# Kernel tuning notes

Measured on AMD Instinct MI355X. Metric: run time of the kernel, lower is better.

Reference implementation:

```python
import jax, jax.numpy as jnp
import numpy as np

IN_F = 4096
OUT_F = 8192
BLOCK = 16   # block_dim
KEEP = 8     # keep_k low-frequency modes kept per block
NLEV = 256   # n_levels


def dct_inv_basis(keep_k, n):
    # Orthonormal DCT-II synthesis basis, rows = kept frequencies k, cols = time index t.
    k = jnp.arange(keep_k, dtype=jnp.float32)[:, None]
    t = jnp.arange(n, dtype=jnp.float32)[None, :]
    B = jnp.cos(jnp.pi * (t + 0.5) * k / n) * jnp.sqrt(2.0 / n)
    scale = jnp.where(jnp.arange(keep_k) == 0, 1.0 / jnp.sqrt(2.0), 1.0)
    return B * scale[:, None]  # [keep_k, block_dim]


def setup_inputs() -> dict:
    key = jax.random.key(0)
    k1, k2, k3, k4, k5 = jax.random.split(key, 5)
    n_blocks = OUT_F * IN_F // BLOCK  # 2097152
    x = jax.random.normal(k1, (32, 8, IN_F), jnp.float32)
    idx = jax.random.randint(k2, (n_blocks, KEEP), 0, NLEV, jnp.int32)
    c_min = jax.random.normal(k3, (KEEP,), jnp.float32)
    c_range = jax.random.uniform(k4, (KEEP,), jnp.float32) + 0.1
    bias = jax.random.normal(k5, (OUT_F,), jnp.float32)
    return {"x": x, "idx": idx, "c_min": c_min, "c_range": c_range, "bias": bias}


def reference(x, idx, c_min, c_range, bias):
    # Affine dequant of kept frequency codes: [n_blocks, keep_k]
    coeffs = idx.astype(jnp.float32) / (NLEV - 1) * c_range + c_min
    # Inverse DCT per block (high-frequency modes are implicitly zero)
    B = dct_inv_basis(KEEP, BLOCK)              # [keep_k, block_dim]
    W = (coeffs @ B).reshape(OUT_F, IN_F)       # dense dequantized weight
    return x @ W.T + bias
```

## Files before the change

kernel.cpp:

```cpp
#include <hip/hip_runtime.h>


typedef __attribute__((ext_vector_type(8))) short bf16x8;
typedef __attribute__((ext_vector_type(4))) float f32x4;

#define K_TOT   2048
#define N_TOT   8192
#define NT      32
#define NCHUNK  8
#define SPC     8
#define LDS_CH  16384

__device__ __forceinline__ unsigned short f2bf_rn(float f) {
    unsigned u = __float_as_uint(f);
    u += 0x7FFFu + ((u >> 16) & 1u);
    return (unsigned short)(u >> 16);
}
__device__ __forceinline__ unsigned pack2(int a, int b) {
    unsigned ua = __float_as_uint((float)a);
    unsigned ub = __float_as_uint((float)b);
    return __builtin_amdgcn_perm(ub, ua, 0x07060302u);
}

__device__ __forceinline__ void lds_barrier() {
    asm volatile("" ::: "memory");
    __builtin_amdgcn_s_waitcnt(0xC07F);
    __builtin_amdgcn_s_barrier();
    asm volatile("" ::: "memory");
}

__global__ __launch_bounds__(256) void prep_kernel(
    const float* __restrict__ x, const float* __restrict__ c_min,
    const float* __restrict__ c_range, unsigned short* __restrict__ Y2f,
    float* __restrict__ corr)
{
    __shared__ float Bk[8][16];
    __shared__ float scmin[8];
    __shared__ float ss[8];
    __shared__ float red[4];
    const int tid = threadIdx.x;
    const int m = blockIdx.x;
    if (tid < 128) {
        int k = tid >> 4, t = tid & 15;
        float v = cosf(3.14159265358979f * (t + 0.5f) * (float)k / 16.0f)
                  * 0.353553390593274f;
        if (k == 0) v *= 0.707106781186548f;
        Bk[k][t] = v;
    }
    if (tid < 8) {
        scmin[tid] = c_min[tid];
        ss[tid] = c_range[tid] * (1.0f / 255.0f);
    }
    __syncthreads();

    const float* xp = x + (long)m * 4096 + tid * 16;
    float xs[16];
#pragma unroll
    for (int q = 0; q < 4; ++q) {
        float4 v = *(const float4*)(xp + q * 4);
        xs[q * 4 + 0] = v.x; xs[q * 4 + 1] = v.y;
        xs[q * 4 + 2] = v.z; xs[q * 4 + 3] = v.w;
    }
    float partial = 0.0f;
    unsigned short yo[8];
#pragma unroll
    for (int k = 0; k < 8; ++k) {
        float y = 0.0f;
#pragma unroll
        for (int t = 0; t < 16; ++t) y += xs[t] * Bk[k][t];
        partial += y * scmin[k];
        yo[k] = f2bf_rn(y * ss[k]);
    }
    uint4 pk;
    pk.x = (unsigned)yo[0] | ((unsigned)yo[1] << 16);
    pk.y = (unsigned)yo[2] | ((unsigned)yo[3] << 16);
    pk.z = (unsigned)yo[4] | ((unsigned)yo[5] << 16);
    pk.w = (unsigned)yo[6] | ((unsigned)yo[7] << 16);
    {
        const int mg = m >> 4, fr = m & 15, kc = tid >> 2, fq = tid & 3;
        unsigned short* dst = Y2f + ((long)((mg * 64 + kc) * 64) + fq * 16 + fr) * 8;
        *(uint4*)dst = pk;
    }
#pragma unroll
    for (int off = 32; off > 0; off >>= 1)
        partial += __shfl_down(partial, off, 64);
    if ((tid & 63) == 0) red[tid >> 6] = partial;
    __syncthreads();
    if (tid == 0) corr[m] = red[0] + red[1] + red[2] + red[3];
}

__global__ __launch_bounds__(256, 2) void gemm_kernel(
    const unsigned short* __restrict__ Y2f, const int* __restrict__ idx,
    const float* __restrict__ bias, const float* __restrict__ corr,
    float* __restrict__ out)
{
    __shared__ char lds[2 * LDS_CH];

    const int tid  = threadIdx.x;
    const int wave = tid >> 6;
    const int lane = tid & 63;
    const int fr   = lane & 15;
    const int fq   = lane >> 4;
    const int o0   = (blockIdx.x & 255) * NT;
    const int h    = blockIdx.x >> 8;

    const int* sBase = idx + (long)(o0 + wave) * K_TOT + lane * 4;
    const int wslot = lane >> 1;
    const int wj    = (lane & 1) * 8;

    const bf16x8* aF[2];
    aF[0] = (const bf16x8*)Y2f + (long)((h * 8 + wave * 2 + 0) * 64) * 64 + lane;
    aF[1] = (const bf16x8*)Y2f + (long)((h * 8 + wave * 2 + 1) * 64) * 64 + lane;

    f32x4 acc[2][2] = {{{0.f,0.f,0.f,0.f},{0.f,0.f,0.f,0.f}},
                       {{0.f,0.f,0.f,0.f},{0.f,0.f,0.f,0.f}}};
    int4 S[8];

#define STAGE_LOAD(ch)                                                    \
    {                                                                     \
        _Pragma("unroll")                                                 \
        for (int l = 0; l < 8; ++l)                                       \
            S[l] = *(const int4*)(sBase + (long)l * 4 * K_TOT + (ch) * 256); \
    }

#define STAGE_WRITE(ch)                                                   \
    {                                                                     \
        char* buf = lds + ((ch) & 1) * LDS_CH;                            \
        _Pragma("unroll")                                                 \
        for (int l = 0; l < 8; ++l) {                                     \
            const int c = wave + l * 4;                                   \
            uint2 w;                                                      \
            w.x = pack2(S[l].x, S[l].y);                                  \
            w.y = pack2(S[l].z, S[l].w);                                  \
            *(uint2*)(buf + c * 512 + ((wslot ^ c) * 16) + wj) = w;       \
        }                                                                 \
    }

#define BREAD(buf, s, g)                                                  \
    (*(const bf16x8*)((buf) + (g * 16 + fr) * 512 +                       \
                      ((((s) * 4 + fq) ^ (g * 16 + fr)) * 16)))

#define COMPUTE(ch)                                                       \
    {                                                                     \
        const char* buf = lds + ((ch) & 1) * LDS_CH;                      \
        bf16x8 a[SPC][2];                                                 \
        _Pragma("unroll")                                                 \
        for (int s = 0; s < SPC; ++s) {                                   \
            a[s][0] = aF[0][((ch) * SPC + s) * 64];                       \
            a[s][1] = aF[1][((ch) * SPC + s) * 64];                       \
        }                                                                 \
        bf16x8 b[2][2];                                                   \
        b[0][0] = BREAD(buf, 0, 0);                                       \
        b[0][1] = BREAD(buf, 0, 1);                                       \
        _Pragma("unroll")                                                 \
        for (int s = 0; s < SPC; ++s) {                                   \
            if (s + 1 < SPC) {                                            \
                b[(s + 1) & 1][0] = BREAD(buf, (s + 1), 0);               \
                b[(s + 1) & 1][1] = BREAD(buf, (s + 1), 1);               \
            }                                                             \
            _Pragma("unroll")                                             \
            for (int mt = 0; mt < 2; ++mt)                                \
                _Pragma("unroll")                                         \
                for (int g = 0; g < 2; ++g)                               \
                    acc[mt][g] = __builtin_amdgcn_mfma_f32_16x16x32_bf16( \
                        a[s][mt], b[s & 1][g], acc[mt][g], 0, 0, 0);      \
        }                                                                 \
    }

    STAGE_LOAD(0)
    STAGE_WRITE(0)
    STAGE_LOAD(1)
    lds_barrier();

#pragma unroll
    for (int c = 0; c < NCHUNK - 2; ++c) {
        COMPUTE(c)
        STAGE_WRITE(c + 1)
        STAGE_LOAD(c + 2)
        lds_barrier();
    }
    COMPUTE(NCHUNK - 2)
    STAGE_WRITE(NCHUNK - 1)
    lds_barrier();
    COMPUTE(NCHUNK - 1)

#pragma unroll
    for (int mt = 0; mt < 2; ++mt) {
#pragma unroll
        for (int g = 0; g < 2; ++g) {
            const int col = o0 + g * 16 + fr;
            const float bv = bias[col];
            const int row0 = (h * 8 + wave * 2 + mt) * 16 + fq * 4;
#pragma unroll
            for (int r = 0; r < 4; ++r)
                out[(long)(row0 + r) * N_TOT + col] =
                    acc[mt][g][r] + bv + corr[row0 + r];
        }
    }
#undef STAGE_LOAD
#undef STAGE_WRITE
#undef BREAD
#undef COMPUTE
}

extern "C" void kernel_launch(void* const* d_in, const int* in_sizes, int n_in,
                              void* d_out, int out_size, void* d_ws, size_t ws_size,
                              hipStream_t stream) {
    const float* x       = (const float*)d_in[0];
    const int*   idx     = (const int*)d_in[1];
    const float* c_min   = (const float*)d_in[2];
    const float* c_range = (const float*)d_in[3];
    const float* bias    = (const float*)d_in[4];
    float* out = (float*)d_out;

    unsigned short* Y2f = (unsigned short*)d_ws;
    float* corr = (float*)((char*)d_ws + (size_t)256 * K_TOT * 2);

    prep_kernel<<<256, 256, 0, stream>>>(x, c_min, c_range, Y2f, corr);
    gemm_kernel<<<512, 256, 0, stream>>>(Y2f, idx, bias, corr, out);
}
```

Measured before the change: 124.5 us.

## Use 512-thread blocks covering all rows so idx codes are converted once

Each block now uses 8 waves that together cover all 256 activation rows for a 32-column output tile. Each idx code is therefore loaded and converted to bf16 once, instead of twice across two half-row blocks. The LDS holds all eight chunks (128 KB), which removes buffer reuse hazards and lets loads run two chunks ahead. The costs are a 256-block grid, which halves the number of blocks, and a large LDS footprint that limits occupancy to one block per CU.

Result: faster. 119.3 us (-4.2%).

```diff
diff --git a/kernel.cpp b/kernel.cpp
--- a/kernel.cpp
+++ b/kernel.cpp
@@ -89,50 +89,50 @@
     if (tid == 0) corr[m] = red[0] + red[1] + red[2] + red[3];
 }
 
-__global__ __launch_bounds__(256, 2) void gemm_kernel(
+__global__ __launch_bounds__(512, 2) void gemm_kernel(
     const unsigned short* __restrict__ Y2f, const int* __restrict__ idx,
     const float* __restrict__ bias, const float* __restrict__ corr,
     float* __restrict__ out)
 {
-    __shared__ char lds[2 * LDS_CH];
+    __shared__ char lds[NCHUNK * LDS_CH];
 
     const int tid  = threadIdx.x;
     const int wave = tid >> 6;
     const int lane = tid & 63;
     const int fr   = lane & 15;
     const int fq   = lane >> 4;
-    const int o0   = (blockIdx.x & 255) * NT;
-    const int h    = blockIdx.x >> 8;
-
-    const int* sBase = idx + (long)(o0 + wave) * K_TOT + lane * 4;
-    const int wslot = lane >> 1;
-    const int wj    = (lane & 1) * 8;
+    const int o0   = blockIdx.x * NT;
+
+    const int scol = tid >> 4;
+    const int skq  = tid & 15;
+    const int* sBase = idx + (long)(o0 + scol) * K_TOT + skq * 4;
 
     const bf16x8* aF[2];
-    aF[0] = (const bf16x8*)Y2f + (long)((h * 8 + wave * 2 + 0) * 64) * 64 + lane;
-    aF[1] = (const bf16x8*)Y2f + (long)((h * 8 + wave * 2 + 1) * 64) * 64 + lane;
+    aF[0] = (const bf16x8*)Y2f + (long)((wave * 2 + 0) * 64) * 64 + lane;
+    aF[1] = (const bf16x8*)Y2f + (long)((wave * 2 + 1) * 64) * 64 + lane;
 
     f32x4 acc[2][2] = {{{0.f,0.f,0.f,0.f},{0.f,0.f,0.f,0.f}},
                        {{0.f,0.f,0.f,0.f},{0.f,0.f,0.f,0.f}}};
-    int4 S[8];
+    int4 S[2][4];
 
 #define STAGE_LOAD(ch)                                                    \
     {                                                                     \
         _Pragma("unroll")                                                 \
-        for (int l = 0; l < 8; ++l)                                       \
-            S[l] = *(const int4*)(sBase + (long)l * 4 * K_TOT + (ch) * 256); \
+        for (int r = 0; r < 4; ++r)                                       \
+            S[(ch) & 1][r] = *(const int4*)(sBase + (ch) * 256 + r * 64); \
     }
 
 #define STAGE_WRITE(ch)                                                   \
     {                                                                     \
-        char* buf = lds + ((ch) & 1) * LDS_CH;                            \
+        char* buf = lds + (ch) * LDS_CH;                                  \
         _Pragma("unroll")                                                 \
-        for (int l = 0; l < 8; ++l) {                                     \
-            const int c = wave + l * 4;                                   \
+        for (int r = 0; r < 4; ++r) {                                     \
+            const int kq = skq + r * 16;                                  \
             uint2 w;                                                      \
-            w.x = pack2(S[l].x, S[l].y);                                  \
-            w.y = pack2(S[l].z, S[l].w);                                  \
-            *(uint2*)(buf + c * 512 + ((wslot ^ c) * 16) + wj) = w;       \
+            w.x = pack2(S[(ch) & 1][r].x, S[(ch) & 1][r].y);              \
+            w.y = pack2(S[(ch) & 1][r].z, S[(ch) & 1][r].w);              \
+            *(uint2*)(buf + scol * 512 + (((kq >> 1) ^ scol) * 16)        \
+                      + (kq & 1) * 8) = w;                                \
         }                                                                 \
     }
 
@@ -140,49 +140,42 @@
     (*(const bf16x8*)((buf) + (g * 16 + fr) * 512 +                       \
                       ((((s) * 4 + fq) ^ (g * 16 + fr)) * 16)))
 
-#define COMPUTE(ch)                                                       \
-    {                                                                     \
-        const char* buf = lds + ((ch) & 1) * LDS_CH;                      \
-        bf16x8 a[SPC][2];                                                 \
-        _Pragma("unroll")                                                 \
-        for (int s = 0; s < SPC; ++s) {                                   \
-            a[s][0] = aF[0][((ch) * SPC + s) * 64];                       \
-            a[s][1] = aF[1][((ch) * SPC + s) * 64];                       \
-        }                                                                 \
-        bf16x8 b[2][2];                                                   \
-        b[0][0] = BREAD(buf, 0, 0);                                       \
-        b[0][1] = BREAD(buf, 0, 1);                                       \
-        _Pragma("unroll")                                                 \
-        for (int s = 0; s < SPC; ++s) {                                   \
-            if (s + 1 < SPC) {                                            \
-                b[(s + 1) & 1][0] = BREAD(buf, (s + 1), 0);               \
-                b[(s + 1) & 1][1] = BREAD(buf, (s + 1), 1);               \
-            }                                                             \
-            _Pragma("unroll")                                             \
-            for (int mt = 0; mt < 2; ++mt)                                \
-                _Pragma("unroll")                                         \
-                for (int g = 0; g < 2; ++g)                               \
-                    acc[mt][g] = __builtin_amdgcn_mfma_f32_16x16x32_bf16( \
-                        a[s][mt], b[s & 1][g], acc[mt][g], 0, 0, 0);      \
-        }                                                                 \
-    }
-
     STAGE_LOAD(0)
+    STAGE_LOAD(1)
     STAGE_WRITE(0)
-    STAGE_LOAD(1)
     lds_barrier();
 
 #pragma unroll
-    for (int c = 0; c < NCHUNK - 2; ++c) {
-        COMPUTE(c)
-        STAGE_WRITE(c + 1)
-        STAGE_LOAD(c + 2)
+    for (int c = 0; c < NCHUNK; ++c) {
+        bf16x8 a[SPC][2];
+#pragma unroll
+        for (int s = 0; s < SPC; ++s) {
+            a[s][0] = aF[0][(c * SPC + s) * 64];
+            a[s][1] = aF[1][(c * SPC + s) * 64];
+        }
+        if (c + 2 < NCHUNK) STAGE_LOAD(c + 2)
+        if (c + 1 < NCHUNK) STAGE_WRITE(c + 1)
         lds_barrier();
-    }
-    COMPUTE(NCHUNK - 2)
-    STAGE_WRITE(NCHUNK - 1)
-    lds_barrier();
-    COMPUTE(NCHUNK - 1)
+        {
+            const char* buf = lds + c * LDS_CH;
+            bf16x8 b[2][2];
+            b[0][0] = BREAD(buf, 0, 0);
+            b[0][1] = BREAD(buf, 0, 1);
+#pragma unroll
+            for (int s = 0; s < SPC; ++s) {
+                if (s + 1 < SPC) {
+                    b[(s + 1) & 1][0] = BREAD(buf, (s + 1), 0);
+                    b[(s + 1) & 1][1] = BREAD(buf, (s + 1), 1);
+                }
+#pragma unroll
+                for (int mt = 0; mt < 2; ++mt)
+#pragma unroll
+                    for (int g = 0; g < 2; ++g)
+                        acc[mt][g] = __builtin_amdgcn_mfma_f32_16x16x32_bf16(
+                            a[s][mt], b[s & 1][g], acc[mt][g], 0, 0, 0);
+            }
+        }
+    }
 
 #pragma unroll
     for (int mt = 0; mt < 2; ++mt) {
@@ -190,7 +183,7 @@
         for (int g = 0; g < 2; ++g) {
             const int col = o0 + g * 16 + fr;
             const float bv = bias[col];
-            const int row0 = (h * 8 + wave * 2 + mt) * 16 + fq * 4;
+            const int row0 = (wave * 2 + mt) * 16 + fq * 4;
 #pragma unroll
             for (int r = 0; r < 4; ++r)
                 out[(long)(row0 + r) * N_TOT + col] =
@@ -200,7 +193,6 @@
 #undef STAGE_LOAD
 #undef STAGE_WRITE
 #undef BREAD
-#undef COMPUTE
 }
 
 extern "C" void kernel_launch(void* const* d_in, const int* in_sizes, int n_in,
@@ -217,5 +209,5 @@
     float* corr = (float*)((char*)d_ws + (size_t)256 * K_TOT * 2);
 
     prep_kernel<<<256, 256, 0, stream>>>(x, c_min, c_range, Y2f, corr);
-    gemm_kernel<<<512, 256, 0, stream>>>(Y2f, idx, bias, corr, out);
-}
+    gemm_kernel<<<256, 512, 0, stream>>>(Y2f, idx, bias, corr, out);
+}
```
